# Performance work log

Hardware: AMD Instinct MI355X
Metric: run time of the kernel (lower is better)

Reference implementation:

```python
import jax, jax.numpy as jnp
import numpy as np

DIM = 1024
HEADS = 16
DIM_HEAD = 64
INNER = HEADS * DIM_HEAD
B, N = 2, 2048


def rope_encoding(seq_len, dim_head):
    inv_freq = 1.0 / (10000.0 ** (jnp.arange(0, dim_head, 2, dtype=jnp.float32) / dim_head))
    pos = jnp.arange(seq_len, dtype=jnp.float32)
    sinusoid = pos[:, None] * inv_freq[None, :]          # [n, d/2]
    return jnp.concatenate([jnp.sin(sinusoid), jnp.cos(sinusoid)], axis=-1)  # [n, d]


def setup_inputs() -> dict:
    key = jax.random.key(0)
    k1, k2, k3, k4 = jax.random.split(key, 4)
    feats = jax.random.normal(k1, (B, N, DIM), dtype=jnp.float32)
    mask = jnp.ones((B, N), dtype=bool)
    # params (torch Linear: y = x @ W.T + b; store as [in, out] for x @ W)
    W_qkv = jax.random.normal(k2, (DIM, 3 * INNER), dtype=jnp.float32) / np.sqrt(DIM)
    W_out = jax.random.normal(k3, (INNER, DIM), dtype=jnp.float32) / np.sqrt(INNER)
    b_out = jax.random.normal(k4, (DIM,), dtype=jnp.float32) * 0.01
    return {"feats": feats, "W_qkv": W_qkv, "W_out": W_out, "b_out": b_out, "mask": mask}


def reference(feats, W_qkv, W_out, b_out, mask):
    b, n, _ = feats.shape
    h, d = HEADS, DIM_HEAD
    scale = d ** -0.5

    qkv = feats @ W_qkv                                   # [b, n, 3*inner]
    q, k, v = jnp.split(qkv, 3, axis=-1)
    to_bhnd = lambda t: t.reshape(b, n, h, d).transpose(0, 2, 1, 3)
    q, k, v = to_bhnd(q), to_bhnd(k), to_bhnd(v)          # [b, h, n, d]

    rope = rope_encoding(n, d)                            # [n, d]
    q = q + rope
    k = k + rope

    m = mask[:, None, :, None]                            # [b, 1, n, 1]
    neg_max = -jnp.finfo(k.dtype).max
    k = jnp.where(m, k, neg_max)

    q = jax.nn.softmax(q, axis=-1)                        # over feature dim
    k = jax.nn.softmax(k, axis=-2)                        # over sequence dim
    q = q * scale
    v = jnp.where(m, v, 0.0)

    context = jnp.einsum('bhnd,bhne->bhde', k, v)         # [b, h, d, d]
    out = jnp.einsum('bhde,bhnd->bhne', context, q)       # [b, h, n, d]
    out = out.transpose(0, 2, 1, 3).reshape(b, n, h * d)  # [b, n, inner]
    out = out @ W_out + b_out                             # [b, n, dim]

    attn = jnp.einsum('bhnd,bhmd->bhnm', q, k) * scale    # [b, h, n, n]
    return out, attn
```

## Files before the change

### kernel.cpp

```cpp
#include <hip/hip_runtime.h>
#include <cstddef>


#define BB     2
#define SEQ    2048
#define DIMM   1024
#define NHEADS 16
#define DH     64
#define TRIPLE 3072
#define ROWS   (BB*SEQ)
#define SCALE  0.125f

typedef unsigned short u16;
typedef unsigned int   u32;
typedef short s16x8 __attribute__((ext_vector_type(8)));
typedef float f32x4 __attribute__((ext_vector_type(4)));
typedef float vf4   __attribute__((ext_vector_type(4)));

static constexpr size_t WS_QB    = 0;
static constexpr size_t WS_KB    = 8388608;
static constexpr size_t WS_DEN   = 16777216;
static constexpr size_t WS_CTX   = 16785408;
static constexpr size_t WS_ROPET = 17309696;
static constexpr size_t WS_AQPK  = 17833984;
static constexpr size_t WS_W2PK  = 34611200;

static constexpr size_t SC_QKV  = 0;
static constexpr size_t SC_APK  = 50331648;
static constexpr size_t SC_WQPK = 67108864;

__device__ __forceinline__ u16 f2bf(float x) {
    u32 u = __float_as_uint(x);
    return (u16)((u + 0x7fffu + ((u >> 16) & 1u)) >> 16);
}
__device__ __forceinline__ float bf2f(u16 h) {
    return __uint_as_float(((u32)h) << 16);
}
__device__ __forceinline__ void glds16(const char* g, char* l) {
    __builtin_amdgcn_global_load_lds(
        (const __attribute__((address_space(1))) void*)g,
        (__attribute__((address_space(3))) void*)l, 16, 0, 0);
}

__device__ __forceinline__ void conv_pack_item(const float* __restrict__ src,
                                               u16* __restrict__ dst, int t)
{
    int g  = t & 3;
    int kb = (t >> 2) & 31;
    int row = t >> 7;
    const float* s = src + (size_t)row * 1024 + kb * 32 + 4 * g;
    float4 xa = *(const float4*)s;
    float4 xb = *(const float4*)(s + 16);
    float xs[8] = {xa.x, xa.y, xa.z, xa.w, xb.x, xb.y, xb.z, xb.w};
    s16x8 hv, lv;
    #pragma unroll
    for (int e = 0; e < 8; ++e) {
        u16 h = f2bf(xs[e]);
        hv[e] = (short)h;
        lv[e] = (short)f2bf(xs[e] - bf2f(h));
    }
    size_t rowc = (size_t)row * 256 + kb * 8;
    int sw = row & 7;
    *(s16x8*)(dst + (rowc + (size_t)(g ^ sw)) * 8)       = hv;
    *(s16x8*)(dst + (rowc + (size_t)((4 | g) ^ sw)) * 8) = lv;
}

__global__ __launch_bounds__(256)
void prologue(float4* __restrict__ denctx, float4* __restrict__ ropeT,
              const float* __restrict__ feats, u16* __restrict__ A_pk,
              const float* __restrict__ Wqkv, u16* __restrict__ Wq_pk)
{
    __shared__ float fb[32][128];
    const int bid = blockIdx.x, tid = threadIdx.x;
    if (bid < 130) {
        denctx[bid * 256 + tid] = float4{0.f, 0.f, 0.f, 0.f};
        return;
    }
    if (bid < 258) {
        int t = (bid - 130) * 256 + tid;
        int pos = t >> 4, r16 = t & 15;
        double a0 = (double)pos * pow(10000.0, -(double)r16 / 32.0);
        double a1 = (double)pos * pow(10000.0, -(double)(r16 + 16) / 32.0);
        float4 v;
        v.x = (float)sin(a0); v.y = (float)sin(a1);
        v.z = (float)cos(a0); v.w = (float)cos(a1);
        ropeT[t] = v;
        return;
    }
    if (bid < 2306) {
        conv_pack_item(feats, A_pk, (bid - 258) * 256 + tid);
        return;
    }
    {
        int cb = bid - 2306;
        int n0 = (cb % 24) * 128, kb = cb / 24, k0 = kb * 32;
        #pragma unroll
        for (int q = 0; q < 4; ++q) {
            int cc = q * 256 + tid;
            int kr = cc >> 5, nc = (cc & 31) * 4;
            *(float4*)&fb[kr][nc] = *(const float4*)&Wqkv[(size_t)(k0 + kr) * TRIPLE + n0 + nc];
        }
        __syncthreads();
        #pragma unroll
        for (int it = 0; it < 2; ++it) {
            int item = it * 256 + tid;
            int g = (item >> 7) & 3, n = item & 127;
            s16x8 hv, lv;
            #pragma unroll
            for (int e = 0; e < 4; ++e) {
                float x0 = fb[4 * g + e][n];
                float x1 = fb[16 + 4 * g + e][n];
                u16 h0 = f2bf(x0), h1 = f2bf(x1);
                hv[e]     = (short)h0;
                hv[e + 4] = (short)h1;
                lv[e]     = (short)f2bf(x0 - bf2f(h0));
                lv[e + 4] = (short)f2bf(x1 - bf2f(h1));
            }
            int row = n0 + n;
            size_t rowc = (size_t)row * 256 + kb * 8;
            int sw = row & 7;
            *(s16x8*)(Wq_pk + (rowc + (size_t)(g ^ sw)) * 8)       = hv;
            *(s16x8*)(Wq_pk + (rowc + (size_t)((4 | g) ^ sw)) * 8) = lv;
        }
    }
}

__global__ __launch_bounds__(256, 3)
void gemm_qkv(const u16* __restrict__ Ap, const u16* __restrict__ Bp,
              float* __restrict__ C, const float* __restrict__ ropeT,
              float* __restrict__ den, u16* __restrict__ qb,
              u16* __restrict__ Aq_pk)
{
    __shared__ __align__(16) char smem[32768];
    const int tid = threadIdx.x;
    const int lane = tid & 63, wid = tid >> 6;
    const int wi = wid >> 1, wj = wid & 1;
    const int r16 = lane & 15, g = lane >> 4;

    const int bid = blockIdx.x;
    const int swz = (bid & 7) * 96 + (bid >> 3);
    const int bx = swz % 24, by = swz / 24;
    const int brow = by * 128, bcol = bx * 128;

    const int srow = wid * 32 + (lane >> 3);
    const int sch  = lane & 7;
    const char* gA = (const char*)Ap + ((size_t)(brow + srow) * 256 + sch) * 16;
    const char* gB = (const char*)Bp + ((size_t)(bcol + srow) * 256 + sch) * 16;
    char* la = smem + wid * 4096;
    char* lb = smem + 16384 + wid * 4096;

    f32x4 acc[4][4] = {};
    size_t koff = 0;
    for (int kb = 0; kb < 32; ++kb, koff += 128) {
        #pragma unroll
        for (int q = 0; q < 4; ++q) {
            glds16(gA + (size_t)q * (8 * 4096) + koff, la + q * 1024);
            glds16(gB + (size_t)q * (8 * 4096) + koff, lb + q * 1024);
        }
        __syncthreads();
        s16x8 ah[4], al[4], bh[4], bl[4];
        #pragma unroll
        for (int i = 0; i < 4; ++i) {
            int ra = wi * 64 + i * 16 + r16;
            const s16x8* Ar = (const s16x8*)(smem + (size_t)ra * 128);
            ah[i] = Ar[g ^ (ra & 7)];
            al[i] = Ar[(4 | g) ^ (ra & 7)];
            int rb = wj * 64 + i * 16 + r16;
            const s16x8* Br = (const s16x8*)(smem + 16384 + (size_t)rb * 128);
            bh[i] = Br[g ^ (rb & 7)];
            bl[i] = Br[(4 | g) ^ (rb & 7)];
        }
        #pragma unroll
        for (int i = 0; i < 4; ++i)
            #pragma unroll
            for (int j = 0; j < 4; ++j) {
                acc[i][j] = __builtin_amdgcn_mfma_f32_16x16x32_bf16(ah[i], bh[j], acc[i][j], 0, 0, 0);
                acc[i][j] = __builtin_amdgcn_mfma_f32_16x16x32_bf16(ah[i], bl[j], acc[i][j], 0, 0, 0);
                acc[i][j] = __builtin_amdgcn_mfma_f32_16x16x32_bf16(al[i], bh[j], acc[i][j], 0, 0, 0);
            }
        __syncthreads();
    }

    const int pos0 = brow & (SEQ - 1);
    const vf4* rT = (const vf4*)ropeT;
    if (bx < 8) {
        const int h = bx * 2 + wj;
        #pragma unroll
        for (int i = 0; i < 4; ++i)
            #pragma unroll
            for (int r = 0; r < 4; ++r) {
                int rloc = wi * 64 + i * 16 + g * 4 + r;
                vf4 rv = rT[(size_t)(pos0 + rloc) * 16 + r16];
                float v[4];
                #pragma unroll
                for (int j = 0; j < 4; ++j) v[j] = acc[i][j][r] + rv[j];
                float m = fmaxf(fmaxf(v[0], v[1]), fmaxf(v[2], v[3]));
                #pragma unroll
                for (int o = 1; o <= 8; o <<= 1) m = fmaxf(m, __shfl_xor(m, o));
                float e[4];
                float s = 0.f;
                #pragma unroll
                for (int j = 0; j < 4; ++j) { e[j] = expf(v[j] - m); s += e[j]; }
                #pragma unroll
                for (int o = 1; o <= 8; o <<= 1) s += __shfl_xor(s, o);
                float inv = SCALE / s;
                int grow = brow + rloc;
                int b = grow >> 11, n = grow & (SEQ - 1);
                size_t qbbase = ((size_t)(b * NHEADS + h) * SEQ + n) * 64;
                int sw = grow & 7;
                size_t aqbase = (size_t)grow * 2048;
                int g2 = r16 >> 2;
                #pragma unroll
                for (int j = 0; j < 4; ++j) {
                    float qv = e[j] * inv;
                    u16 hi = f2bf(qv);
                    u16 lo = f2bf(qv - bf2f(hi));
                    int db = j >> 1;
                    int elem = (r16 & 3) + 4 * (j & 1);
                    qb[qbbase + db * 32 + g2 * 8 + elem] = hi;
                    size_t ab = aqbase + (size_t)(h * 2 + db) * 64;
                    Aq_pk[ab + ((g2 ^ sw) * 8 + elem)]       = hi;
                    Aq_pk[ab + (((4 | g2) ^ sw) * 8 + elem)] = lo;
                }
            }
    } else if (bx < 16) {
        float dsum[4] = {0.f, 0.f, 0.f, 0.f};
        #pragma unroll
        for (int i = 0; i < 4; ++i)
            #pragma unroll
            for (int r = 0; r < 4; ++r) {
                int rloc = wi * 64 + i * 16 + g * 4 + r;
                vf4 rv = rT[(size_t)(pos0 + rloc) * 16 + r16];
                size_t rb = (size_t)(brow + rloc) * TRIPLE + bcol + wj * 64;
                #pragma unroll
                for (int j = 0; j < 4; ++j) {
                    float e = expf(acc[i][j][r] + rv[j]);
                    C[rb + j * 16 + r16] = e;
                    dsum[j] += e;
                }
            }
        const int bD = (brow >> 11) * DIMM;
        #pragma unroll
        for (int j = 0; j < 4; ++j) {
            float s = dsum[j];
            s += __shfl_xor(s, 16);
            s += __shfl_xor(s, 32);
            if (g == 0)
                atomicAdd(&den[bD + (bcol - DIMM) + wj * 64 + j * 16 + r16], s);
        }
    } else {
        #pragma unroll
        for (int i = 0; i < 4; ++i) {
            int row = brow + wi * 64 + i * 16 + g * 4;
            #pragma unroll
            for (int j = 0; j < 4; ++j) {
                int col = bcol + wj * 64 + j * 16 + r16;
                #pragma unroll
                for (int r = 0; r < 4; ++r)
                    C[(size_t)(row + r) * TRIPLE + col] = acc[i][j][r];
            }
        }
    }
}

__global__ __launch_bounds__(256)
void packctx(const float* __restrict__ qkv, const float* __restrict__ den,
             u16* __restrict__ kb, float* __restrict__ ctx)
{
    __shared__ float kt[32][64];
    __shared__ float vt[32][64];
    if (blockIdx.x < 512) {
        int t = blockIdx.x * 256 + threadIdx.x;
        int db = t & 1;
        int h  = (t >> 1) & 15;
        int row = t >> 5;
        int b = row >> 11, n = row & (SEQ - 1);
        size_t dst = ((size_t)(b * NHEADS + h) * SEQ + n) * 64 + db * 32;
        const float* sk = qkv + (size_t)row * TRIPLE + DIMM + h * DH + db * 32;
        const float* dn = den + (size_t)b * DIMM + h * DH + db * 32;
        #pragma unroll
        for (int g = 0; g < 4; ++g) {
            float4 xa = *(const float4*)(sk + 4 * g);
            float4 xb = *(const float4*)(sk + 16 + 4 * g);
            float4 da = *(const float4*)(dn + 4 * g);
            float4 dc = *(const float4*)(dn + 16 + 4 * g);
            float xs[8] = {xa.x / da.x, xa.y / da.y, xa.z / da.z, xa.w / da.w,
                           xb.x / dc.x, xb.y / dc.y, xb.z / dc.z, xb.w / dc.w};
            s16x8 hv;
            #pragma unroll
            for (int e = 0; e < 8; ++e) hv[e] = (short)f2bf(xs[e]);
            *(s16x8*)(kb + dst + g * 8) = hv;
        }
        return;
    }
    int cb = blockIdx.x - 512;
    int chunk = cb & 7, h = (cb >> 3) & 15, b = cb >> 7;
    int row0 = b * SEQ + chunk * 256;
    int d  = threadIdx.x & 63;
    int eg = threadIdx.x >> 6;
    float acc[16] = {};
    for (int t = 0; t < 8; ++t) {
        #pragma unroll
        for (int q = 0; q < 2; ++q) {
            int lf = threadIdx.x * 2 + q;
            int nn = lf >> 4;
            int c4 = (lf & 15) * 4;
            size_t base = (size_t)(row0 + t * 32 + nn) * TRIPLE + DIMM + h * DH + c4;
            *(float4*)&kt[nn][c4] = *(const float4*)&qkv[base];
            *(float4*)&vt[nn][c4] = *(const float4*)&qkv[base + DIMM];
        }
        __syncthreads();
        #pragma unroll 8
        for (int nn = 0; nn < 32; ++nn) {
            float kv = kt[nn][d];
            #pragma unroll
            for (int j = 0; j < 16; ++j)
                acc[j] = fmaf(kv, vt[nn][eg * 16 + j], acc[j]);
        }
        __syncthreads();
    }
    float rden = 1.f / den[(size_t)b * DIMM + h * DH + d];
    size_t cbase = ((size_t)(b * NHEADS + h)) * (DH * DH) + d * DH + eg * 16;
    #pragma unroll
    for (int j = 0; j < 16; ++j) atomicAdd(&ctx[cbase + j], acc[j] * rden);
}

__global__ __launch_bounds__(256)
void W2k(const float* __restrict__ ctx, const float* __restrict__ Wout,
         u16* __restrict__ W2_pk)
{
    __shared__ float cl[64][64];
    const int bid = blockIdx.x, tid = threadIdx.x;
    const int ct = bid & 7, h = (bid >> 3) & 15, b = bid >> 7;
    const float* C = ctx + ((size_t)(b * NHEADS + h)) * (DH * DH);
    for (int i = tid; i < DH * DH; i += 256) cl[i >> 6][i & 63] = C[i];
    __syncthreads();
    const int c = ct * 128 + (tid & 127);
    const int dg = tid >> 7;
    float acc[32] = {};
    for (int e = 0; e < 64; ++e) {
        float wv = Wout[(size_t)(h * 64 + e) * DIMM + c];
        #pragma unroll
        for (int r = 0; r < 32; ++r)
            acc[r] = fmaf(cl[dg * 32 + r][e], wv, acc[r]);
    }
    s16x8 hv[4], lv[4];
    #pragma unroll
    for (int r = 0; r < 32; ++r) {
        int g2 = (r & 15) >> 2;
        int elem = (r & 3) + 4 * (r >> 4);
        u16 hh = f2bf(acc[r]);
        hv[g2][elem] = (short)hh;
        lv[g2][elem] = (short)f2bf(acc[r] - bf2f(hh));
    }
    const int sw = c & 7;
    u16* base = W2_pk + (size_t)b * 2097152 + (size_t)c * 2048 + (size_t)(h * 2 + dg) * 64;
    #pragma unroll
    for (int g2 = 0; g2 < 4; ++g2) {
        *(s16x8*)(base + ((g2 ^ sw) * 8))       = hv[g2];
        *(s16x8*)(base + (((4 | g2) ^ sw) * 8)) = lv[g2];
    }
}

__global__ __launch_bounds__(256, 2)
void epilogue2(const u16* __restrict__ Aq_pk, const u16* __restrict__ W2_pk,
               float* __restrict__ outp, const float* __restrict__ bias,
               const u16* __restrict__ qb, const u16* __restrict__ kb,
               float* __restrict__ attn)
{
    __shared__ __align__(16) char smem[65536];
    const int tid = threadIdx.x;
    const int lane = tid & 63, wid = tid >> 6;
    const int r16 = lane & 15, g = lane >> 4;
    const int bid = blockIdx.x;

    if (bid < 1536 && bid % 3 == 0) {
        const int gb = bid / 3;
        const int wi = wid >> 1, wj = wid & 1;
        const int swz = (gb & 7) * 64 + (gb >> 3);
        const int bx = swz >> 6, by = swz & 63;
        const int brow = by * 64, bcol = bx * 128;
        const int srA = wid * 16 + (lane >> 3);
        const int srB = wid * 32 + (lane >> 3);
        const int sch = lane & 7;
        const char* gA = (const char*)Aq_pk + ((size_t)(brow + srA) * 256 + sch) * 16;
        const char* gB = (const char*)(W2_pk + (size_t)(brow >> 11) * 2097152)
                         + ((size_t)(bcol + srB) * 256 + sch) * 16;

        auto STAGE = [&](int buf, int kb2) {
            size_t koff = (size_t)kb2 * 128;
            char* a = smem + buf * 24576 + wid * 2048;
            char* b = smem + buf * 24576 + 8192 + wid * 4096;
            #pragma unroll
            for (int q = 0; q < 2; ++q)
                glds16(gA + (size_t)q * (8 * 4096) + koff, a + q * 1024);
            #pragma unroll
            for (int q = 0; q < 4; ++q)
                glds16(gB + (size_t)q * (8 * 4096) + koff, b + q * 1024);
        };

        f32x4 acc[2][4] = {};
        STAGE(0, 0);
        __syncthreads();
        for (int kb2 = 0; kb2 < 32; ++kb2) {
            const int cur = kb2 & 1;
            if (kb2 < 31) STAGE(cur ^ 1, kb2 + 1);
            const char* Ab = smem + cur * 24576;
            const char* Bb = smem + cur * 24576 + 8192;
            s16x8 ah[2], al[2], bh[4], bl[4];
            #pragma unroll
            for (int i = 0; i < 2; ++i) {
                int ra = wi * 32 + i * 16 + r16;
                const s16x8* Ar = (const s16x8*)(Ab + (size_t)ra * 128);
                ah[i] = Ar[g ^ (ra & 7)];
                al[i] = Ar[(4 | g) ^ (ra & 7)];
            }
            #pragma unroll
            for (int j = 0; j < 4; ++j) {
                int rb = wj * 64 + j * 16 + r16;
                const s16x8* Br = (const s16x8*)(Bb + (size_t)rb * 128);
                bh[j] = Br[g ^ (rb & 7)];
                bl[j] = Br[(4 | g) ^ (rb & 7)];
            }
            #pragma unroll
            for (int i = 0; i < 2; ++i)
                #pragma unroll
                for (int j = 0; j < 4; ++j) {
                    acc[i][j] = __builtin_amdgcn_mfma_f32_16x16x32_bf16(ah[i], bh[j], acc[i][j], 0, 0, 0);
                    acc[i][j] = __builtin_amdgcn_mfma_f32_16x16x32_bf16(ah[i], bl[j], acc[i][j], 0, 0, 0);
                    acc[i][j] = __builtin_amdgcn_mfma_f32_16x16x32_bf16(al[i], bh[j], acc[i][j], 0, 0, 0);
                }
            __syncthreads();
        }
        #pragma unroll
        for (int i = 0; i < 2; ++i) {
            int row = brow + wi * 32 + i * 16 + g * 4;
            #pragma unroll
            for (int j = 0; j < 4; ++j) {
                int col = bcol + wj * 64 + j * 16 + r16;
                float bv = bias[col];
                #pragma unroll
                for (int r = 0; r < 4; ++r)
                    outp[(size_t)(row + r) * DIMM + col] = acc[i][j][r] + bv;
            }
        }
        return;
    }

    const int ab = (bid < 1536) ? (bid - bid / 3 - 1) : (1024 + bid - 1536);
    const int bh = ab >> 8;
    const int n0 = ((ab >> 4) & 15) * 128, m0 = (ab & 15) * 128;
    const int wi = wid >> 1, wj = wid & 1;
    float* ost = (float*)smem;
    const u16* qB = qb + (size_t)bh * (SEQ * 64);
    const u16* kB = kb + (size_t)bh * (SEQ * 64);
    f32x4 acc[4][4] = {};
    #pragma unroll
    for (int db = 0; db < 2; ++db) {
        s16x8 a[4], b[4];
        #pragma unroll
        for (int i = 0; i < 4; ++i) {
            a[i] = *(const s16x8*)(qB + (size_t)(n0 + wi * 64 + i * 16 + r16) * 64 + db * 32 + g * 8);
            b[i] = *(const s16x8*)(kB + (size_t)(m0 + wj * 64 + i * 16 + r16) * 64 + db * 32 + g * 8);
        }
        #pragma unroll
        for (int i = 0; i < 4; ++i)
            #pragma unroll
            for (int j = 0; j < 4; ++j)
                acc[i][j] = __builtin_amdgcn_mfma_f32_16x16x32_bf16(a[i], b[j], acc[i][j], 0, 0, 0);
    }
    #pragma unroll
    for (int i = 0; i < 4; ++i)
        #pragma unroll
        for (int j = 0; j < 4; ++j)
            #pragma unroll
            for (int r = 0; r < 4; ++r)
                ost[(wi * 64 + i * 16 + g * 4 + r) * 128 + wj * 64 + j * 16 + r16] =
                    acc[i][j][r] * SCALE;
    __syncthreads();
    size_t base = (size_t)bh * ((size_t)SEQ * SEQ) + (size_t)n0 * SEQ + m0;
    int rr = tid >> 5, c16 = tid & 31;
    #pragma unroll
    for (int it = 0; it < 16; ++it) {
        int row = rr * 16 + it;
        vf4 v = *(vf4*)&ost[row * 128 + c16 * 4];
        __builtin_nontemporal_store(v, (vf4*)&attn[base + (size_t)row * SEQ + c16 * 4]);
    }
}

extern "C" void kernel_launch(void* const* d_in, const int* in_sizes, int n_in,
                              void* d_out, int out_size, void* d_ws, size_t ws_size,
                              hipStream_t stream)
{
    const float* feats = (const float*)d_in[0];
    const float* Wqkv  = (const float*)d_in[1];
    const float* Wout  = (const float*)d_in[2];
    const float* bout  = (const float*)d_in[3];

    char*  wsb   = (char*)d_ws;
    u16*   qb    = (u16*)(wsb + WS_QB);
    u16*   kb    = (u16*)(wsb + WS_KB);
    float* den   = (float*)(wsb + WS_DEN);
    float* ctx   = (float*)(wsb + WS_CTX);
    float* ropeT = (float*)(wsb + WS_ROPET);
    u16*   Aq_pk = (u16*)(wsb + WS_AQPK);
    u16*   W2_pk = (u16*)(wsb + WS_W2PK);

    float* out  = (float*)d_out;
    float* attn = out + (size_t)ROWS * DIMM;
    char*  sc   = (char*)attn;
    float* qkv   = (float*)(sc + SC_QKV);
    u16*   A_pk  = (u16*)(sc + SC_APK);
    u16*   Wq_pk = (u16*)(sc + SC_WQPK);

    prologue<<<3074, 256, 0, stream>>>((float4*)den, (float4*)ropeT,
                                       feats, A_pk, Wqkv, Wq_pk);
    gemm_qkv<<<768, 256, 0, stream>>>(A_pk, Wq_pk, qkv, ropeT, den, qb, Aq_pk);
    packctx<<<768, 256, 0, stream>>>(qkv, den, kb, ctx);
    W2k<<<256, 256, 0, stream>>>(ctx, Wout, W2_pk);
    epilogue2<<<8704, 256, 0, stream>>>(Aq_pk, W2_pk, out, bout, qb, kb, attn);
}
```

Before: 318.7 us.

## Store exp(K) and V as bf16 head-major buffers instead of fp32 qkv

The QKV GEMM epilogue now writes exp(K+rope) and V directly as bf16 in a per-head [b,h,n,64] layout, with K permuted to match the later fragment order, instead of storing a full fp32 row-major qkv matrix. The packctx kernel reads these half-size, contiguous buffers for both K normalisation and the K^T V context reduction, and un-permutes the d index when writing ctx. This halves intermediate traffic and makes the reads coalesced per head. The cost is scattered 2-byte global stores in the GEMM epilogue and an extra bf16 rounding of exp(K) before division by the denominator, which changes precision.

New measurement: 335.2 us. 5.2% more time.

```diff
diff --git a/kernel.cpp b/kernel.cpp
--- a/kernel.cpp
+++ b/kernel.cpp
@@ -25,7 +25,8 @@
 static constexpr size_t WS_AQPK  = 17833984;
 static constexpr size_t WS_W2PK  = 34611200;
 
-static constexpr size_t SC_QKV  = 0;
+static constexpr size_t SC_KBU  = 0;
+static constexpr size_t SC_VB   = 8388608;
 static constexpr size_t SC_APK  = 50331648;
 static constexpr size_t SC_WQPK = 67108864;
 
@@ -127,9 +128,9 @@
 
 __global__ __launch_bounds__(256, 3)
 void gemm_qkv(const u16* __restrict__ Ap, const u16* __restrict__ Bp,
-              float* __restrict__ C, const float* __restrict__ ropeT,
-              float* __restrict__ den, u16* __restrict__ qb,
-              u16* __restrict__ Aq_pk)
+              const float* __restrict__ ropeT, float* __restrict__ den,
+              u16* __restrict__ qb, u16* __restrict__ Aq_pk,
+              u16* __restrict__ kbu, u16* __restrict__ vb)
 {
     __shared__ __align__(16) char smem[32768];
     const int tid = threadIdx.x;
@@ -231,12 +232,17 @@
             for (int r = 0; r < 4; ++r) {
                 int rloc = wi * 64 + i * 16 + g * 4 + r;
                 vf4 rv = rT[(size_t)(pos0 + rloc) * 16 + r16];
-                size_t rb = (size_t)(brow + rloc) * TRIPLE + bcol + wj * 64;
+                int grow = brow + rloc;
+                int b = grow >> 11, n = grow & (SEQ - 1);
                 #pragma unroll
                 for (int j = 0; j < 4; ++j) {
                     float e = expf(acc[i][j][r] + rv[j]);
-                    C[rb + j * 16 + r16] = e;
                     dsum[j] += e;
+                    int d1024 = (bcol - DIMM) + wj * 64 + j * 16 + r16;
+                    int h = d1024 >> 6, d = d1024 & 63;
+                    int db = d >> 5, dd = d & 31;
+                    int sg = ((dd & 15) >> 2) * 8 + (dd & 3) + ((dd >> 4) << 2);
+                    kbu[((size_t)(b * NHEADS + h) * SEQ + n) * 64 + db * 32 + sg] = f2bf(e);
                 }
             }
         const int bD = (brow >> 11) * DIMM;
@@ -250,77 +256,91 @@
         }
     } else {
         #pragma unroll
-        for (int i = 0; i < 4; ++i) {
-            int row = brow + wi * 64 + i * 16 + g * 4;
-            #pragma unroll
-            for (int j = 0; j < 4; ++j) {
-                int col = bcol + wj * 64 + j * 16 + r16;
-                #pragma unroll
-                for (int r = 0; r < 4; ++r)
-                    C[(size_t)(row + r) * TRIPLE + col] = acc[i][j][r];
-            }
-        }
+        for (int i = 0; i < 4; ++i)
+            #pragma unroll
+            for (int r = 0; r < 4; ++r) {
+                int rloc = wi * 64 + i * 16 + g * 4 + r;
+                int grow = brow + rloc;
+                int b = grow >> 11, n = grow & (SEQ - 1);
+                #pragma unroll
+                for (int j = 0; j < 4; ++j) {
+                    int e1024 = (bcol - 2 * DIMM) + wj * 64 + j * 16 + r16;
+                    int h = e1024 >> 6, e = e1024 & 63;
+                    vb[((size_t)(b * NHEADS + h) * SEQ + n) * 64 + e] = f2bf(acc[i][j][r]);
+                }
+            }
     }
 }
 
 __global__ __launch_bounds__(256)
-void packctx(const float* __restrict__ qkv, const float* __restrict__ den,
-             u16* __restrict__ kb, float* __restrict__ ctx)
-{
-    __shared__ float kt[32][64];
-    __shared__ float vt[32][64];
+void packctx(const u16* __restrict__ kbu, const u16* __restrict__ vb,
+             const float* __restrict__ den, u16* __restrict__ kb,
+             float* __restrict__ ctx)
+{
+    __shared__ __align__(16) u16 kt[32][64];
+    __shared__ __align__(16) u16 vt[32][64];
     if (blockIdx.x < 512) {
         int t = blockIdx.x * 256 + threadIdx.x;
         int db = t & 1;
         int h  = (t >> 1) & 15;
         int row = t >> 5;
         int b = row >> 11, n = row & (SEQ - 1);
-        size_t dst = ((size_t)(b * NHEADS + h) * SEQ + n) * 64 + db * 32;
-        const float* sk = qkv + (size_t)row * TRIPLE + DIMM + h * DH + db * 32;
+        size_t off = ((size_t)(b * NHEADS + h) * SEQ + n) * 64 + db * 32;
         const float* dn = den + (size_t)b * DIMM + h * DH + db * 32;
         #pragma unroll
         for (int g = 0; g < 4; ++g) {
-            float4 xa = *(const float4*)(sk + 4 * g);
-            float4 xb = *(const float4*)(sk + 16 + 4 * g);
+            s16x8 kv = *(const s16x8*)(kbu + off + g * 8);
             float4 da = *(const float4*)(dn + 4 * g);
             float4 dc = *(const float4*)(dn + 16 + 4 * g);
-            float xs[8] = {xa.x / da.x, xa.y / da.y, xa.z / da.z, xa.w / da.w,
-                           xb.x / dc.x, xb.y / dc.y, xb.z / dc.z, xb.w / dc.w};
             s16x8 hv;
-            #pragma unroll
-            for (int e = 0; e < 8; ++e) hv[e] = (short)f2bf(xs[e]);
-            *(s16x8*)(kb + dst + g * 8) = hv;
+            hv[0] = (short)f2bf(bf2f((u16)kv[0]) / da.x);
+            hv[1] = (short)f2bf(bf2f((u16)kv[1]) / da.y);
+            hv[2] = (short)f2bf(bf2f((u16)kv[2]) / da.z);
+            hv[3] = (short)f2bf(bf2f((u16)kv[3]) / da.w);
+            hv[4] = (short)f2bf(bf2f((u16)kv[4]) / dc.x);
+            hv[5] = (short)f2bf(bf2f((u16)kv[5]) / dc.y);
+            hv[6] = (short)f2bf(bf2f((u16)kv[6]) / dc.z);
+            hv[7] = (short)f2bf(bf2f((u16)kv[7]) / dc.w);
+            *(s16x8*)(kb + off + g * 8) = hv;
         }
         return;
     }
     int cb = blockIdx.x - 512;
     int chunk = cb & 7, h = (cb >> 3) & 15, b = cb >> 7;
-    int row0 = b * SEQ + chunk * 256;
-    int d  = threadIdx.x & 63;
+    int bh = b * NHEADS + h;
+    const u16* kB = kbu + (size_t)bh * (SEQ * 64);
+    const u16* vB = vb  + (size_t)bh * (SEQ * 64);
+    int n0 = chunk * 256;
+    int p  = threadIdx.x & 63;
     int eg = threadIdx.x >> 6;
     float acc[16] = {};
     for (int t = 0; t < 8; ++t) {
         #pragma unroll
         for (int q = 0; q < 2; ++q) {
-            int lf = threadIdx.x * 2 + q;
-            int nn = lf >> 4;
-            int c4 = (lf & 15) * 4;
-            size_t base = (size_t)(row0 + t * 32 + nn) * TRIPLE + DIMM + h * DH + c4;
-            *(float4*)&kt[nn][c4] = *(const float4*)&qkv[base];
-            *(float4*)&vt[nn][c4] = *(const float4*)&qkv[base + DIMM];
+            int u = q * 256 + threadIdx.x;
+            if (u < 256) {
+                int nn = u >> 3, c8 = (u & 7) * 8;
+                *(s16x8*)&kt[nn][c8] = *(const s16x8*)(kB + (size_t)(n0 + t * 32 + nn) * 64 + c8);
+            } else {
+                int uu = u - 256;
+                int nn = uu >> 3, c8 = (uu & 7) * 8;
+                *(s16x8*)&vt[nn][c8] = *(const s16x8*)(vB + (size_t)(n0 + t * 32 + nn) * 64 + c8);
+            }
         }
         __syncthreads();
         #pragma unroll 8
         for (int nn = 0; nn < 32; ++nn) {
-            float kv = kt[nn][d];
+            float kval = bf2f(kt[nn][p]);
             #pragma unroll
             for (int j = 0; j < 16; ++j)
-                acc[j] = fmaf(kv, vt[nn][eg * 16 + j], acc[j]);
+                acc[j] = fmaf(kval, bf2f(vt[nn][eg * 16 + j]), acc[j]);
         }
         __syncthreads();
     }
+    int pp = p & 31;
+    int d = (p >> 5) * 32 + 4 * (pp >> 3) + (pp & 3) + ((pp >> 2) & 1) * 16;
     float rden = 1.f / den[(size_t)b * DIMM + h * DH + d];
-    size_t cbase = ((size_t)(b * NHEADS + h)) * (DH * DH) + d * DH + eg * 16;
+    size_t cbase = (size_t)bh * (DH * DH) + (size_t)d * DH + eg * 16;
     #pragma unroll
     for (int j = 0; j < 16; ++j) atomicAdd(&ctx[cbase + j], acc[j] * rden);
 }
@@ -509,14 +529,15 @@
     float* out  = (float*)d_out;
     float* attn = out + (size_t)ROWS * DIMM;
     char*  sc   = (char*)attn;
-    float* qkv   = (float*)(sc + SC_QKV);
+    u16*   kbu   = (u16*)(sc + SC_KBU);
+    u16*   vb    = (u16*)(sc + SC_VB);
     u16*   A_pk  = (u16*)(sc + SC_APK);
     u16*   Wq_pk = (u16*)(sc + SC_WQPK);
 
     prologue<<<3074, 256, 0, stream>>>((float4*)den, (float4*)ropeT,
                                        feats, A_pk, Wqkv, Wq_pk);
-    gemm_qkv<<<768, 256, 0, stream>>>(A_pk, Wq_pk, qkv, ropeT, den, qb, Aq_pk);
-    packctx<<<768, 256, 0, stream>>>(qkv, den, kb, ctx);
+    gemm_qkv<<<768, 256, 0, stream>>>(A_pk, Wq_pk, ropeT, den, qb, Aq_pk, kbu, vb);
+    packctx<<<768, 256, 0, stream>>>(kbu, vb, den, kb, ctx);
     W2k<<<256, 256, 0, stream>>>(ctx, Wout, W2_pk);
     epilogue2<<<8704, 256, 0, stream>>>(Aq_pk, W2_pk, out, bout, qb, kb, attn);
 }
```
